# Kernel tuning notes

Measured on AMD Instinct MI355X. Metric: run time of the kernel, lower is better.

The kernel has to match this reference:

```python
import jax, jax.numpy as jnp
import numpy as np
from jax import lax

H = 1024
E = 8
TOP_K = 2


def setup_inputs() -> dict:
    key = jax.random.key(0)
    kx, k1, k2 = jax.random.split(key, 3)
    x = jax.random.normal(kx, (8, 2048, H), dtype=jnp.float32)
    # router MLP params, init normal(0, 0.02), zero bias (matches _init_weights)
    w1 = jax.random.normal(k1, (H, 2 * H), dtype=jnp.float32) * 0.02
    b1 = jnp.zeros((2 * H,), dtype=jnp.float32)
    w2 = jax.random.normal(k2, (2 * H, E), dtype=jnp.float32) * 0.02
    b2 = jnp.zeros((E,), dtype=jnp.float32)
    return {"x": x, "w1": w1, "b1": b1, "w2": w2, "b2": b2}


def reference(x, w1, b1, w2, b2):
    # gating MLP: Linear -> GELU (exact, torch default) -> Linear
    h = jax.nn.gelu(jnp.einsum('bsh,hf->bsf', x, w1) + b1, approximate=False)
    expert_weights = jnp.einsum('bsf,fe->bse', h, w2) + b2  # [B,S,E]

    top_k_weights, top_k_indices = lax.top_k(expert_weights, TOP_K)  # [B,S,K]
    top_k_weights = jax.nn.softmax(top_k_weights, axis=-1)

    # scatter renormalized weights into dense [B,S,E] mask (indices distinct -> one-hot sum)
    onehot = jax.nn.one_hot(top_k_indices, E, dtype=expert_weights.dtype)  # [B,S,K,E]
    masks = jnp.einsum('bsk,bske->bse', top_k_weights, onehot)

    expert_usage = masks.sum(axis=(0, 1))
    expert_usage = expert_usage / expert_usage.sum()
    target_usage = jnp.full_like(expert_usage, 1.0 / E)
    load_balancing_loss = jnp.mean((expert_usage - target_usage) ** 2)

    sparsity_loss = jnp.mean(jnp.sum(masks > 0, axis=-1).astype(jnp.float32)) / TOP_K
    total_loss = load_balancing_loss + 0.1 * sparsity_loss

    return expert_weights, masks, total_loss, expert_usage
```

## Files before the change

kernel.cpp:

```cpp
#include <hip/hip_runtime.h>
#include <math.h>

#define HDIM 1024
#define FDIM 2048
#define NEXP 8
#define MTOK 16384
#define NSLC 32
#define BM 128
#define BN 128

typedef __attribute__((ext_vector_type(8))) short bf16x8;
typedef __attribute__((ext_vector_type(4))) float f32x4;

__device__ inline unsigned short f2bf_rne(float f) {
    unsigned int u = __float_as_uint(f);
    u = (u + 0x7FFFu + ((u >> 16) & 1u)) >> 16;
    return (unsigned short)u;
}
__device__ inline float bf2f(unsigned short h) {
    unsigned int u = ((unsigned int)h) << 16;
    return __uint_as_float(u);
}

__global__ __launch_bounds__(256) void cvt_x(const float* __restrict__ x,
                                             unsigned short* __restrict__ af)
{
    __shared__ unsigned short hs[16384];
    __shared__ unsigned short ls[16384];
    const int mt = blockIdx.x;
    const float* src = x + (size_t)mt * 16384;
    const int m = threadIdx.x & 15;
    const int kseg = threadIdx.x >> 4;

    #pragma unroll
    for (int c = 0; c < 8; c++) {
        int k = c * 128 + kseg * 8;
        float v[8];
        *(float4*)(v)     = *(const float4*)(src + m * 1024 + k);
        *(float4*)(v + 4) = *(const float4*)(src + m * 1024 + k + 4);
        union { unsigned short u[8]; uint4 q; } oh, ol;
        #pragma unroll
        for (int j = 0; j < 8; j++) {
            unsigned short h = f2bf_rne(v[j]);
            oh.u[j] = h;
            ol.u[j] = f2bf_rne(v[j] - bf2f(h));
        }
        int kb = k >> 5, q = (k >> 3) & 3;
        int o = kb * 512 + m * 32 + q * 8;
        *(uint4*)(hs + o) = oh.q;
        *(uint4*)(ls + o) = ol.q;
    }
    __syncthreads();
    unsigned short* dst = af + (size_t)mt * 32768;
    #pragma unroll
    for (int c = 0; c < 16; c++) {
        int f = c * 2048 + threadIdx.x * 8;
        int kb = f >> 10, half = (f >> 9) & 1, idx = f & 511;
        int q = idx >> 7, mm = (idx >> 3) & 15;
        const unsigned short* s = (half ? ls : hs) + kb * 512 + mm * 32 + q * 8;
        *(uint4*)(dst + f) = *(const uint4*)s;
    }
}

__global__ __launch_bounds__(256) void cvt_w1f(const float* __restrict__ w1,
                                               unsigned short* __restrict__ wf)
{
    __shared__ float t[32][33];
    int n0 = blockIdx.x * 32;
    int k0 = blockIdx.y * 32;
    int lx = threadIdx.x & 31, ly = threadIdx.x >> 5;
    #pragma unroll
    for (int r = 0; r < 32; r += 8)
        t[ly + r][lx] = w1[(size_t)(k0 + ly + r) * FDIM + n0 + lx];
    __syncthreads();
    #pragma unroll
    for (int r = 0; r < 32; r += 8) {
        float v = t[lx][ly + r];
        unsigned short h = f2bf_rne(v);
        unsigned short l = f2bf_rne(v - bf2f(h));
        int n = n0 + ly + r, k = k0 + lx;
        size_t base = (size_t)((n >> 4) * 32 + (k >> 5)) * 1024;
        int lj = (((k >> 3) & 3) * 16 + (n & 15)) * 8 + (k & 7);
        wf[base + lj] = h;
        wf[base + 512 + lj] = l;
    }
}

__global__ __launch_bounds__(256, 2) void gemm1_mfma(
    const unsigned short* __restrict__ af, const unsigned short* __restrict__ wf,
    const float* __restrict__ b1, const float* __restrict__ w2,
    float* __restrict__ part)
{
    const int tid  = threadIdx.x;
    const int lane = tid & 63;
    const int l15  = lane & 15;
    const int q    = lane >> 4;
    const int wave = tid >> 6;
    const int wm   = wave & 1;
    const int wn   = wave >> 1;

    const int id = blockIdx.x;
    const int xcd = id & 7, seq = id >> 3;
    const int strip = seq >> 6;
    const int bn = (seq >> 2) & 15;
    const int bmo = seq & 3;
    const int bm = strip * 32 + xcd * 4 + bmo;
    const int m0 = bm * BM, n0 = bn * BN;

    const unsigned short* apt[4];
    const unsigned short* bpt[4];
    #pragma unroll
    for (int i = 0; i < 4; i++) {
        apt[i] = af + ((size_t)(bm * 8 + wm * 4 + i) * 32) * 1024 + lane * 8;
        bpt[i] = wf + ((size_t)(bn * 8 + wn * 4 + i) * 32) * 1024 + lane * 8;
    }

    f32x4 acc[4][4];
    #pragma unroll
    for (int i = 0; i < 4; i++)
        #pragma unroll
        for (int j = 0; j < 4; j++) acc[i][j] = (f32x4){0.f, 0.f, 0.f, 0.f};

    bf16x8 Ah0[4], Al0[4], Bh0[4], Bl0[4];
    bf16x8 Ah1[4], Al1[4], Bh1[4], Bl1[4];

    #pragma unroll
    for (int i = 0; i < 4; i++) {
        Ah0[i] = *(const bf16x8*)(apt[i]);
        Al0[i] = *(const bf16x8*)(apt[i] + 512);
        Bh0[i] = *(const bf16x8*)(bpt[i]);
        Bl0[i] = *(const bf16x8*)(bpt[i] + 512);
    }

    #pragma unroll 1
    for (int t = 0; t < 32; t += 2) {
        #pragma unroll
        for (int i = 0; i < 4; i++) {
            Ah1[i] = *(const bf16x8*)(apt[i] + 1024);
            Al1[i] = *(const bf16x8*)(apt[i] + 1536);
            Bh1[i] = *(const bf16x8*)(bpt[i] + 1024);
            Bl1[i] = *(const bf16x8*)(bpt[i] + 1536);
        }
        #pragma unroll
        for (int i = 0; i < 4; i++)
            #pragma unroll
            for (int j = 0; j < 4; j++) {
                acc[i][j] = __builtin_amdgcn_mfma_f32_16x16x32_bf16(
                    Ah0[i], Bh0[j], acc[i][j], 0, 0, 0);
                acc[i][j] = __builtin_amdgcn_mfma_f32_16x16x32_bf16(
                    Ah0[i], Bl0[j], acc[i][j], 0, 0, 0);
                acc[i][j] = __builtin_amdgcn_mfma_f32_16x16x32_bf16(
                    Al0[i], Bh0[j], acc[i][j], 0, 0, 0);
            }
        #pragma unroll
        for (int i = 0; i < 4; i++) { apt[i] += 2048; bpt[i] += 2048; }
        if (t + 2 < 32) {
            #pragma unroll
            for (int i = 0; i < 4; i++) {
                Ah0[i] = *(const bf16x8*)(apt[i]);
                Al0[i] = *(const bf16x8*)(apt[i] + 512);
                Bh0[i] = *(const bf16x8*)(bpt[i]);
                Bl0[i] = *(const bf16x8*)(bpt[i] + 512);
            }
        }
        #pragma unroll
        for (int i = 0; i < 4; i++)
            #pragma unroll
            for (int j = 0; j < 4; j++) {
                acc[i][j] = __builtin_amdgcn_mfma_f32_16x16x32_bf16(
                    Ah1[i], Bh1[j], acc[i][j], 0, 0, 0);
                acc[i][j] = __builtin_amdgcn_mfma_f32_16x16x32_bf16(
                    Ah1[i], Bl1[j], acc[i][j], 0, 0, 0);
                acc[i][j] = __builtin_amdgcn_mfma_f32_16x16x32_bf16(
                    Al1[i], Bh1[j], acc[i][j], 0, 0, 0);
            }
    }

    #pragma unroll
    for (int j = 0; j < 4; j++) {
        int n = n0 + wn * 64 + j * 16 + l15;
        float bb = b1[n];
        #pragma unroll
        for (int i = 0; i < 4; i++)
            #pragma unroll
            for (int r = 0; r < 4; r++) {
                float v = acc[i][j][r] + bb;
                acc[i][j][r] = 0.5f * v * (1.0f + erff(v * 0.70710678118654752f));
            }
    }

    float w2r[4][8];
    #pragma unroll
    for (int j = 0; j < 4; j++) {
        const float4* p = (const float4*)(w2 + (size_t)(n0 + wn * 64 + j * 16 + l15) * NEXP);
        float4 u = p[0], v = p[1];
        w2r[j][0] = u.x; w2r[j][1] = u.y; w2r[j][2] = u.z; w2r[j][3] = u.w;
        w2r[j][4] = v.x; w2r[j][5] = v.y; w2r[j][6] = v.z; w2r[j][7] = v.w;
    }

    const int sl = bn * 2 + wn;
    #pragma unroll
    for (int e = 0; e < NEXP; e++) {
        float p[4][4];
        #pragma unroll
        for (int i = 0; i < 4; i++)
            #pragma unroll
            for (int r = 0; r < 4; r++) {
                float s = 0.f;
                #pragma unroll
                for (int j = 0; j < 4; j++) s += acc[i][j][r] * w2r[j][e];
                p[i][r] = s;
            }
        #pragma unroll
        for (int off = 1; off < 16; off <<= 1)
            #pragma unroll
            for (int i = 0; i < 4; i++)
                #pragma unroll
                for (int r = 0; r < 4; r++)
                    p[i][r] += __shfl_xor(p[i][r], off);
        if (l15 == 0) {
            #pragma unroll
            for (int i = 0; i < 4; i++)
                #pragma unroll
                for (int r = 0; r < 4; r++) {
                    int m = m0 + wm * 64 + i * 16 + q * 4 + r;
                    part[(size_t)sl * (MTOK * NEXP) + (size_t)m * NEXP + e] = p[i][r];
                }
        }
    }
}

__global__ __launch_bounds__(256) void router_topk(
    const float* __restrict__ part, const float* __restrict__ b2,
    float* __restrict__ out, float* __restrict__ gu, int* __restrict__ gc)
{
    const int t = blockIdx.x * 256 + threadIdx.x;

    float logit[8];
    #pragma unroll
    for (int e = 0; e < 8; e++) logit[e] = b2[e];
    #pragma unroll
    for (int j = 0; j < NSLC; j++) {
        const float4* p4 = (const float4*)(part + (size_t)j * (MTOK * NEXP) + (size_t)t * NEXP);
        float4 u = p4[0], v = p4[1];
        logit[0] += u.x; logit[1] += u.y; logit[2] += u.z; logit[3] += u.w;
        logit[4] += v.x; logit[5] += v.y; logit[6] += v.z; logit[7] += v.w;
    }

    int i1 = 0; float v1 = logit[0];
    #pragma unroll
    for (int e = 1; e < 8; e++) { if (logit[e] > v1) { v1 = logit[e]; i1 = e; } }
    int i2 = -1; float v2 = -INFINITY;
    #pragma unroll
    for (int e = 0; e < 8; e++) {
        if (e != i1 && logit[e] > v2) { v2 = logit[e]; i2 = e; }
    }
    float ex = expf(v2 - v1);
    float inv = 1.0f / (1.0f + ex);
    float wa = inv, wb = ex * inv;

    float4* o = (float4*)(out + (size_t)t * NEXP);
    o[0] = make_float4(logit[0], logit[1], logit[2], logit[3]);
    o[1] = make_float4(logit[4], logit[5], logit[6], logit[7]);

    float mk[8];
    #pragma unroll
    for (int e = 0; e < 8; e++) mk[e] = 0.0f;
    mk[i1] = wa; mk[i2] = wb;
    float4* om = (float4*)(out + (size_t)(MTOK * NEXP) + (size_t)t * NEXP);
    om[0] = make_float4(mk[0], mk[1], mk[2], mk[3]);
    om[1] = make_float4(mk[4], mk[5], mk[6], mk[7]);

    __shared__ float us[8];
    __shared__ int cs;
    if (threadIdx.x < 8) us[threadIdx.x] = 0.0f;
    if (threadIdx.x == 0) cs = 0;
    __syncthreads();
    atomicAdd(&us[i1], wa);
    atomicAdd(&us[i2], wb);
    int cnt = (wa > 0.0f ? 1 : 0) + (wb > 0.0f ? 1 : 0);
    atomicAdd(&cs, cnt);
    __syncthreads();
    if (threadIdx.x < 8) atomicAdd(&gu[threadIdx.x], us[threadIdx.x]);
    if (threadIdx.x == 0) atomicAdd(gc, cs);
}

__global__ void router_final(const float* __restrict__ gu, const int* __restrict__ gc,
                             float* __restrict__ out)
{
    if (blockIdx.x == 0 && threadIdx.x == 0) {
        float u[8]; float tot = 0.0f;
        for (int e = 0; e < 8; e++) { u[e] = gu[e]; tot += u[e]; }
        float lb = 0.0f;
        for (int e = 0; e < 8; e++) {
            float un = u[e] / tot;
            out[2 * MTOK * NEXP + 1 + e] = un;
            float d = un - 0.125f;
            lb += d * d;
        }
        lb *= (1.0f / 8.0f);
        float sp = ((float)(*gc) / (float)MTOK) * 0.5f;
        out[2 * MTOK * NEXP] = lb + 0.1f * sp;
    }
}

extern "C" void kernel_launch(void* const* d_in, const int* in_sizes, int n_in,
                              void* d_out, int out_size, void* d_ws, size_t ws_size,
                              hipStream_t stream) {
    const float* x  = (const float*)d_in[0];
    const float* w1 = (const float*)d_in[1];
    const float* b1 = (const float*)d_in[2];
    const float* w2 = (const float*)d_in[3];
    const float* b2 = (const float*)d_in[4];
    float* out = (float*)d_out;

    unsigned short* af = (unsigned short*)d_ws;
    unsigned short* wf = af + (size_t)1024 * 32768;
    float* part = (float*)(wf + (size_t)128 * 32 * 1024);
    float* gu = part + (size_t)NSLC * MTOK * NEXP;
    int* gc = (int*)(gu + 8);

    hipMemsetAsync(gu, 0, 64, stream);

    cvt_x<<<1024, 256, 0, stream>>>(x, af);
    cvt_w1f<<<dim3(FDIM / 32, HDIM / 32), 256, 0, stream>>>(w1, wf);
    gemm1_mfma<<<2048, 256, 0, stream>>>(af, wf, b1, w2, part);
    router_topk<<<MTOK / 256, 256, 0, stream>>>(part, b2, out, gu, gc);
    router_final<<<1, 64, 0, stream>>>(gu, gc, out);
}
```

Before: 343.2 us.

## Stage GEMM tiles through LDS with a triple-buffered async global_load_lds pipeline

The gate GEMM moves from per-wave direct global-to-register loads to block-wide async global_load_lds copies into a three-stage LDS ring. Tiles grow to 256x128, with 512 threads and 8 waves per block. Every operand tile is now fetched once per block and shared by all waves, which cuts redundant global and L2 traffic and overlaps loads with MFMA work. The cost is about 144KB of dynamic LDS, which allows only one block per CU, plus barriers on every k-step and a setprio hint.

```diff
diff --git a/kernel.cpp b/kernel.cpp
--- a/kernel.cpp
+++ b/kernel.cpp
@@ -6,8 +6,8 @@
 #define NEXP 8
 #define MTOK 16384
 #define NSLC 32
-#define BM 128
-#define BN 128
+#define LDSB 24576
+#define LDS_BYTES (3 * 49152)
 
 typedef __attribute__((ext_vector_type(8))) short bf16x8;
 typedef __attribute__((ext_vector_type(4))) float f32x4;
@@ -86,33 +86,42 @@
     }
 }
 
-__global__ __launch_bounds__(256, 2) void gemm1_mfma(
+#define GLDX4(gp, lofs) __builtin_amdgcn_global_load_lds( \
+    (const __attribute__((address_space(1))) unsigned int*)(uintptr_t)(gp), \
+    (__attribute__((address_space(3))) unsigned int*)(unsigned int)(uintptr_t)(smem + (lofs)), \
+    16, 0, 0)
+
+__global__ __launch_bounds__(512, 2) void gemm1_mfma(
     const unsigned short* __restrict__ af, const unsigned short* __restrict__ wf,
     const float* __restrict__ b1, const float* __restrict__ w2,
     float* __restrict__ part)
 {
+    extern __shared__ unsigned short smem[];
     const int tid  = threadIdx.x;
     const int lane = tid & 63;
     const int l15  = lane & 15;
     const int q    = lane >> 4;
     const int wave = tid >> 6;
-    const int wm   = wave & 1;
-    const int wn   = wave >> 1;
-
-    const int id = blockIdx.x;
+    const int wm   = wave >> 1;
+    const int wn   = wave & 1;
+
+    const int id  = blockIdx.x;
     const int xcd = id & 7, seq = id >> 3;
-    const int strip = seq >> 6;
-    const int bn = (seq >> 2) & 15;
-    const int bmo = seq & 3;
-    const int bm = strip * 32 + xcd * 4 + bmo;
-    const int m0 = bm * BM, n0 = bn * BN;
-
-    const unsigned short* apt[4];
-    const unsigned short* bpt[4];
-    #pragma unroll
-    for (int i = 0; i < 4; i++) {
-        apt[i] = af + ((size_t)(bm * 8 + wm * 4 + i) * 32) * 1024 + lane * 8;
-        bpt[i] = wf + ((size_t)(bn * 8 + wn * 4 + i) * 32) * 1024 + lane * 8;
+    const int bn  = seq & 15;
+    const int bm  = xcd * 8 + (seq >> 4);
+    const int m0  = bm * 256, n0g = bn * 128;
+
+    const unsigned short* gb[6];
+    int lo[6];
+    #pragma unroll
+    for (int s = 0; s < 6; s++) {
+        int c = wave * 6 + s;
+        int f = c >> 1, half = c & 1;
+        const unsigned short* base = (f < 16)
+            ? af + (size_t)(bm * 16 + f) * 32768
+            : wf + (size_t)(bn * 8 + (f - 16)) * 32768;
+        gb[s] = base + half * 512 + lane * 8;
+        lo[s] = f * 1024 + half * 512;
     }
 
     f32x4 acc[4][4];
@@ -121,64 +130,58 @@
         #pragma unroll
         for (int j = 0; j < 4; j++) acc[i][j] = (f32x4){0.f, 0.f, 0.f, 0.f};
 
-    bf16x8 Ah0[4], Al0[4], Bh0[4], Bl0[4];
-    bf16x8 Ah1[4], Al1[4], Bh1[4], Bl1[4];
-
-    #pragma unroll
-    for (int i = 0; i < 4; i++) {
-        Ah0[i] = *(const bf16x8*)(apt[i]);
-        Al0[i] = *(const bf16x8*)(apt[i] + 512);
-        Bh0[i] = *(const bf16x8*)(bpt[i]);
-        Bl0[i] = *(const bf16x8*)(bpt[i] + 512);
-    }
-
+    #pragma unroll
+    for (int s = 0; s < 6; s++) GLDX4(gb[s], lo[s]);
+    #pragma unroll
+    for (int s = 0; s < 6; s++) GLDX4(gb[s] + 1024, LDSB + lo[s]);
+    asm volatile("s_waitcnt vmcnt(6)\n\ts_barrier" ::: "memory");
+
+    int bo = 0;
     #pragma unroll 1
-    for (int t = 0; t < 32; t += 2) {
-        #pragma unroll
-        for (int i = 0; i < 4; i++) {
-            Ah1[i] = *(const bf16x8*)(apt[i] + 1024);
-            Al1[i] = *(const bf16x8*)(apt[i] + 1536);
-            Bh1[i] = *(const bf16x8*)(bpt[i] + 1024);
-            Bl1[i] = *(const bf16x8*)(bpt[i] + 1536);
-        }
-        #pragma unroll
-        for (int i = 0; i < 4; i++)
-            #pragma unroll
-            for (int j = 0; j < 4; j++) {
-                acc[i][j] = __builtin_amdgcn_mfma_f32_16x16x32_bf16(
-                    Ah0[i], Bh0[j], acc[i][j], 0, 0, 0);
-                acc[i][j] = __builtin_amdgcn_mfma_f32_16x16x32_bf16(
-                    Ah0[i], Bl0[j], acc[i][j], 0, 0, 0);
-                acc[i][j] = __builtin_amdgcn_mfma_f32_16x16x32_bf16(
-                    Al0[i], Bh0[j], acc[i][j], 0, 0, 0);
+    for (int t = 0; t < 32; t++) {
+        int bi = bo + 2 * LDSB; if (bi >= 3 * LDSB) bi -= 3 * LDSB;
+        if (t + 2 < 32) {
+            #pragma unroll
+            for (int s = 0; s < 6; s++)
+                GLDX4(gb[s] + (size_t)(t + 2) * 1024, bi + lo[s]);
+        }
+        const unsigned short* sb = smem + bo;
+        bf16x8 Bh[4], Bl[4];
+        #pragma unroll
+        for (int j = 0; j < 4; j++) {
+            Bh[j] = *(const bf16x8*)(sb + (16 + wn * 4 + j) * 1024 + lane * 8);
+            Bl[j] = *(const bf16x8*)(sb + (16 + wn * 4 + j) * 1024 + 512 + lane * 8);
+        }
+        __builtin_amdgcn_s_setprio(1);
+        #pragma unroll
+        for (int ih = 0; ih < 2; ih++) {
+            bf16x8 Ah[2], Al[2];
+            #pragma unroll
+            for (int i = 0; i < 2; i++) {
+                int mt = wm * 4 + ih * 2 + i;
+                Ah[i] = *(const bf16x8*)(sb + mt * 1024 + lane * 8);
+                Al[i] = *(const bf16x8*)(sb + mt * 1024 + 512 + lane * 8);
             }
-        #pragma unroll
-        for (int i = 0; i < 4; i++) { apt[i] += 2048; bpt[i] += 2048; }
-        if (t + 2 < 32) {
-            #pragma unroll
-            for (int i = 0; i < 4; i++) {
-                Ah0[i] = *(const bf16x8*)(apt[i]);
-                Al0[i] = *(const bf16x8*)(apt[i] + 512);
-                Bh0[i] = *(const bf16x8*)(bpt[i]);
-                Bl0[i] = *(const bf16x8*)(bpt[i] + 512);
-            }
-        }
-        #pragma unroll
-        for (int i = 0; i < 4; i++)
-            #pragma unroll
-            for (int j = 0; j < 4; j++) {
-                acc[i][j] = __builtin_amdgcn_mfma_f32_16x16x32_bf16(
-                    Ah1[i], Bh1[j], acc[i][j], 0, 0, 0);
-                acc[i][j] = __builtin_amdgcn_mfma_f32_16x16x32_bf16(
-                    Ah1[i], Bl1[j], acc[i][j], 0, 0, 0);
-                acc[i][j] = __builtin_amdgcn_mfma_f32_16x16x32_bf16(
-                    Al1[i], Bh1[j], acc[i][j], 0, 0, 0);
-            }
+            #pragma unroll
+            for (int i = 0; i < 2; i++)
+                #pragma unroll
+                for (int j = 0; j < 4; j++) {
+                    f32x4 a = acc[ih * 2 + i][j];
+                    a = __builtin_amdgcn_mfma_f32_16x16x32_bf16(Ah[i], Bh[j], a, 0, 0, 0);
+                    a = __builtin_amdgcn_mfma_f32_16x16x32_bf16(Ah[i], Bl[j], a, 0, 0, 0);
+                    a = __builtin_amdgcn_mfma_f32_16x16x32_bf16(Al[i], Bh[j], a, 0, 0, 0);
+                    acc[ih * 2 + i][j] = a;
+                }
+        }
+        __builtin_amdgcn_s_setprio(0);
+        bo += LDSB; if (bo >= 3 * LDSB) bo -= 3 * LDSB;
+        if (t < 30)       asm volatile("s_waitcnt vmcnt(6)\n\ts_barrier" ::: "memory");
+        else if (t == 30) asm volatile("s_waitcnt vmcnt(0)\n\ts_barrier" ::: "memory");
     }
 
     #pragma unroll
     for (int j = 0; j < 4; j++) {
-        int n = n0 + wn * 64 + j * 16 + l15;
+        int n = n0g + wn * 64 + j * 16 + l15;
         float bb = b1[n];
         #pragma unroll
         for (int i = 0; i < 4; i++)
@@ -192,7 +195,7 @@
     float w2r[4][8];
     #pragma unroll
     for (int j = 0; j < 4; j++) {
-        const float4* p = (const float4*)(w2 + (size_t)(n0 + wn * 64 + j * 16 + l15) * NEXP);
+        const float4* p = (const float4*)(w2 + (size_t)(n0g + wn * 64 + j * 16 + l15) * NEXP);
         float4 u = p[0], v = p[1];
         w2r[j][0] = u.x; w2r[j][1] = u.y; w2r[j][2] = u.z; w2r[j][3] = u.w;
         w2r[j][4] = v.x; w2r[j][5] = v.y; w2r[j][6] = v.z; w2r[j][7] = v.w;
@@ -320,11 +323,18 @@
     float* gu = part + (size_t)NSLC * MTOK * NEXP;
     int* gc = (int*)(gu + 8);
 
+    static bool attr_done = false;
+    if (!attr_done) {
+        hipFuncSetAttribute((const void*)gemm1_mfma,
+                            hipFuncAttributeMaxDynamicSharedMemorySize, LDS_BYTES);
+        attr_done = true;
+    }
+
     hipMemsetAsync(gu, 0, 64, stream);
 
     cvt_x<<<1024, 256, 0, stream>>>(x, af);
     cvt_w1f<<<dim3(FDIM / 32, HDIM / 32), 256, 0, stream>>>(w1, wf);
-    gemm1_mfma<<<2048, 256, 0, stream>>>(af, wf, b1, w2, part);
+    gemm1_mfma<<<1024, 512, LDS_BYTES, stream>>>(af, wf, b1, w2, part);
     router_topk<<<MTOK / 256, 256, 0, stream>>>(part, b2, out, gu, gc);
     router_final<<<1, 64, 0, stream>>>(gu, gc, out);
 }
```

New measurement: 360.5 us. 1.05x slower.

## Cut operand register footprint in split-bf16 GEMM to raise occupancy to three blocks

Applied to the files above, without the earlier changes.

The main loop no longer double-buffers the low-half bf16 operands. It keeps a single Al/Bl buffer that is reloaded just before use, and reorders the MFMAs so all hi*hi products run before the cross terms. The launch bound rises from 2 to 3 blocks per CU, which fits the smaller register set and gives more waves to hide latency. In exchange, the low-half loads have less time to arrive before their MFMAs need them, which may expose global load latency.

```diff
diff --git a/kernel.cpp b/kernel.cpp
--- a/kernel.cpp
+++ b/kernel.cpp
@@ -86,7 +86,7 @@
     }
 }
 
-__global__ __launch_bounds__(256, 2) void gemm1_mfma(
+__global__ __launch_bounds__(256, 3) void gemm1_mfma(
     const unsigned short* __restrict__ af, const unsigned short* __restrict__ wf,
     const float* __restrict__ b1, const float* __restrict__ w2,
     float* __restrict__ part)
@@ -121,59 +121,72 @@
         #pragma unroll
         for (int j = 0; j < 4; j++) acc[i][j] = (f32x4){0.f, 0.f, 0.f, 0.f};
 
-    bf16x8 Ah0[4], Al0[4], Bh0[4], Bl0[4];
-    bf16x8 Ah1[4], Al1[4], Bh1[4], Bl1[4];
+    bf16x8 Ah0[4], Bh0[4];
+    bf16x8 Ah1[4], Bh1[4];
+    bf16x8 Al[4],  Bl[4];
 
     #pragma unroll
     for (int i = 0; i < 4; i++) {
         Ah0[i] = *(const bf16x8*)(apt[i]);
-        Al0[i] = *(const bf16x8*)(apt[i] + 512);
         Bh0[i] = *(const bf16x8*)(bpt[i]);
-        Bl0[i] = *(const bf16x8*)(bpt[i] + 512);
     }
 
     #pragma unroll 1
     for (int t = 0; t < 32; t += 2) {
         #pragma unroll
         for (int i = 0; i < 4; i++) {
+            Al[i] = *(const bf16x8*)(apt[i] + 512);
+            Bl[i] = *(const bf16x8*)(bpt[i] + 512);
+        }
+        #pragma unroll
+        for (int i = 0; i < 4; i++) {
             Ah1[i] = *(const bf16x8*)(apt[i] + 1024);
-            Al1[i] = *(const bf16x8*)(apt[i] + 1536);
             Bh1[i] = *(const bf16x8*)(bpt[i] + 1024);
-            Bl1[i] = *(const bf16x8*)(bpt[i] + 1536);
-        }
+        }
+        #pragma unroll
+        for (int i = 0; i < 4; i++)
+            #pragma unroll
+            for (int j = 0; j < 4; j++)
+                acc[i][j] = __builtin_amdgcn_mfma_f32_16x16x32_bf16(
+                    Ah0[i], Bh0[j], acc[i][j], 0, 0, 0);
         #pragma unroll
         for (int i = 0; i < 4; i++)
             #pragma unroll
             for (int j = 0; j < 4; j++) {
                 acc[i][j] = __builtin_amdgcn_mfma_f32_16x16x32_bf16(
-                    Ah0[i], Bh0[j], acc[i][j], 0, 0, 0);
-                acc[i][j] = __builtin_amdgcn_mfma_f32_16x16x32_bf16(
-                    Ah0[i], Bl0[j], acc[i][j], 0, 0, 0);
-                acc[i][j] = __builtin_amdgcn_mfma_f32_16x16x32_bf16(
-                    Al0[i], Bh0[j], acc[i][j], 0, 0, 0);
+                    Ah0[i], Bl[j], acc[i][j], 0, 0, 0);
+                acc[i][j] = __builtin_amdgcn_mfma_f32_16x16x32_bf16(
+                    Al[i], Bh0[j], acc[i][j], 0, 0, 0);
+            }
+        #pragma unroll
+        for (int i = 0; i < 4; i++) {
+            Al[i] = *(const bf16x8*)(apt[i] + 1536);
+            Bl[i] = *(const bf16x8*)(bpt[i] + 1536);
+        }
+        if (t + 2 < 32) {
+            #pragma unroll
+            for (int i = 0; i < 4; i++) {
+                Ah0[i] = *(const bf16x8*)(apt[i] + 2048);
+                Bh0[i] = *(const bf16x8*)(bpt[i] + 2048);
+            }
+        }
+        #pragma unroll
+        for (int i = 0; i < 4; i++)
+            #pragma unroll
+            for (int j = 0; j < 4; j++)
+                acc[i][j] = __builtin_amdgcn_mfma_f32_16x16x32_bf16(
+                    Ah1[i], Bh1[j], acc[i][j], 0, 0, 0);
+        #pragma unroll
+        for (int i = 0; i < 4; i++)
+            #pragma unroll
+            for (int j = 0; j < 4; j++) {
+                acc[i][j] = __builtin_amdgcn_mfma_f32_16x16x32_bf16(
+                    Ah1[i], Bl[j], acc[i][j], 0, 0, 0);
+                acc[i][j] = __builtin_amdgcn_mfma_f32_16x16x32_bf16(
+                    Al[i], Bh1[j], acc[i][j], 0, 0, 0);
             }
         #pragma unroll
         for (int i = 0; i < 4; i++) { apt[i] += 2048; bpt[i] += 2048; }
-        if (t + 2 < 32) {
-            #pragma unroll
-            for (int i = 0; i < 4; i++) {
-                Ah0[i] = *(const bf16x8*)(apt[i]);
-                Al0[i] = *(const bf16x8*)(apt[i] + 512);
-                Bh0[i] = *(const bf16x8*)(bpt[i]);
-                Bl0[i] = *(const bf16x8*)(bpt[i] + 512);
-            }
-        }
-        #pragma unroll
-        for (int i = 0; i < 4; i++)
-            #pragma unroll
-            for (int j = 0; j < 4; j++) {
-                acc[i][j] = __builtin_amdgcn_mfma_f32_16x16x32_bf16(
-                    Ah1[i], Bh1[j], acc[i][j], 0, 0, 0);
-                acc[i][j] = __builtin_amdgcn_mfma_f32_16x16x32_bf16(
-                    Ah1[i], Bl1[j], acc[i][j], 0, 0, 0);
-                acc[i][j] = __builtin_amdgcn_mfma_f32_16x16x32_bf16(
-                    Al1[i], Bh1[j], acc[i][j], 0, 0, 0);
-            }
     }
 
     #pragma unroll
```

Result: slower. 383.2 us (+11.6%).

## Enlarge GEMM1 block tile to 256x128 with interleaved A-fragment streaming

Applied to the files above, without the earlier changes.

The GEMM block tile in M doubles from 128 to 256 rows, so each wave holds 8x4 accumulators and every loaded B fragment feeds twice as many MFMAs. The grid halves to 1024 blocks and the block-to-XCD mapping changes. The K loop is rescheduled so A fragments stream in pairs, interleaved with MFMA groups, while B fragments for the next k-step are prefetched, which keeps register pressure bounded. The goal is to cut global/L2 load traffic per MFMA, at the cost of more accumulator registers (a risk to the two-blocks-per-SIMD occupancy target) and fewer blocks to balance across CUs.

```diff
diff --git a/kernel.cpp b/kernel.cpp
--- a/kernel.cpp
+++ b/kernel.cpp
@@ -6,8 +6,6 @@
 #define NEXP 8
 #define MTOK 16384
 #define NSLC 32
-#define BM 128
-#define BN 128
 
 typedef __attribute__((ext_vector_type(8))) short bf16x8;
 typedef __attribute__((ext_vector_type(4))) float f32x4;
@@ -86,6 +84,34 @@
     }
 }
 
+#define LOADB(BH, BL, tt) do { \
+    _Pragma("unroll") \
+    for (int j_ = 0; j_ < 4; j_++) { \
+        const unsigned short* p_ = bbase + (size_t)j_ * 32768 + (size_t)(tt) * 1024; \
+        BH[j_] = *(const bf16x8*)(p_); \
+        BL[j_] = *(const bf16x8*)(p_ + 512); \
+    } } while (0)
+
+#define LOADA(AH, AL, ip, tt) do { \
+    _Pragma("unroll") \
+    for (int k_ = 0; k_ < 2; k_++) { \
+        const unsigned short* p_ = abase + (size_t)((ip) * 2 + k_) * 32768 + (size_t)(tt) * 1024; \
+        AH[k_] = *(const bf16x8*)(p_); \
+        AL[k_] = *(const bf16x8*)(p_ + 512); \
+    } } while (0)
+
+#define MFMA_PAIR(AH, AL, BH, BL, ip) do { \
+    _Pragma("unroll") \
+    for (int k_ = 0; k_ < 2; k_++) \
+        _Pragma("unroll") \
+        for (int j_ = 0; j_ < 4; j_++) { \
+            f32x4 a_ = acc[(ip) * 2 + k_][j_]; \
+            a_ = __builtin_amdgcn_mfma_f32_16x16x32_bf16(AH[k_], BH[j_], a_, 0, 0, 0); \
+            a_ = __builtin_amdgcn_mfma_f32_16x16x32_bf16(AH[k_], BL[j_], a_, 0, 0, 0); \
+            a_ = __builtin_amdgcn_mfma_f32_16x16x32_bf16(AL[k_], BH[j_], a_, 0, 0, 0); \
+            acc[(ip) * 2 + k_][j_] = a_; \
+        } } while (0)
+
 __global__ __launch_bounds__(256, 2) void gemm1_mfma(
     const unsigned short* __restrict__ af, const unsigned short* __restrict__ wf,
     const float* __restrict__ b1, const float* __restrict__ w2,
@@ -99,81 +125,49 @@
     const int wm   = wave & 1;
     const int wn   = wave >> 1;
 
-    const int id = blockIdx.x;
+    const int id  = blockIdx.x;
     const int xcd = id & 7, seq = id >> 3;
-    const int strip = seq >> 6;
-    const int bn = (seq >> 2) & 15;
-    const int bmo = seq & 3;
-    const int bm = strip * 32 + xcd * 4 + bmo;
-    const int m0 = bm * BM, n0 = bn * BN;
-
-    const unsigned short* apt[4];
-    const unsigned short* bpt[4];
-    #pragma unroll
-    for (int i = 0; i < 4; i++) {
-        apt[i] = af + ((size_t)(bm * 8 + wm * 4 + i) * 32) * 1024 + lane * 8;
-        bpt[i] = wf + ((size_t)(bn * 8 + wn * 4 + i) * 32) * 1024 + lane * 8;
-    }
-
-    f32x4 acc[4][4];
-    #pragma unroll
-    for (int i = 0; i < 4; i++)
+    const int bn  = seq & 15;
+    const int bm  = xcd * 8 + (seq >> 4);
+    const int m0  = bm * 256, n0 = bn * 128;
+
+    const unsigned short* abase = af + (size_t)(bm * 16 + wm * 8) * 32768 + lane * 8;
+    const unsigned short* bbase = wf + (size_t)(bn * 8 + wn * 4) * 32768 + lane * 8;
+
+    f32x4 acc[8][4];
+    #pragma unroll
+    for (int i = 0; i < 8; i++)
         #pragma unroll
         for (int j = 0; j < 4; j++) acc[i][j] = (f32x4){0.f, 0.f, 0.f, 0.f};
 
-    bf16x8 Ah0[4], Al0[4], Bh0[4], Bl0[4];
-    bf16x8 Ah1[4], Al1[4], Bh1[4], Bl1[4];
-
-    #pragma unroll
-    for (int i = 0; i < 4; i++) {
-        Ah0[i] = *(const bf16x8*)(apt[i]);
-        Al0[i] = *(const bf16x8*)(apt[i] + 512);
-        Bh0[i] = *(const bf16x8*)(bpt[i]);
-        Bl0[i] = *(const bf16x8*)(bpt[i] + 512);
-    }
+    bf16x8 BhA[4], BlA[4], BhB[4], BlB[4];
+    bf16x8 AhX[2], AlX[2], AhY[2], AlY[2];
+
+    LOADB(BhA, BlA, 0);
+    LOADA(AhX, AlX, 0, 0);
 
     #pragma unroll 1
     for (int t = 0; t < 32; t += 2) {
-        #pragma unroll
-        for (int i = 0; i < 4; i++) {
-            Ah1[i] = *(const bf16x8*)(apt[i] + 1024);
-            Al1[i] = *(const bf16x8*)(apt[i] + 1536);
-            Bh1[i] = *(const bf16x8*)(bpt[i] + 1024);
-            Bl1[i] = *(const bf16x8*)(bpt[i] + 1536);
+        LOADA(AhY, AlY, 1, t);
+        MFMA_PAIR(AhX, AlX, BhA, BlA, 0);
+        LOADA(AhX, AlX, 2, t);
+        MFMA_PAIR(AhY, AlY, BhA, BlA, 1);
+        LOADA(AhY, AlY, 3, t);
+        MFMA_PAIR(AhX, AlX, BhA, BlA, 2);
+        LOADB(BhB, BlB, t + 1);
+        LOADA(AhX, AlX, 0, t + 1);
+        MFMA_PAIR(AhY, AlY, BhA, BlA, 3);
+        LOADA(AhY, AlY, 1, t + 1);
+        MFMA_PAIR(AhX, AlX, BhB, BlB, 0);
+        LOADA(AhX, AlX, 2, t + 1);
+        MFMA_PAIR(AhY, AlY, BhB, BlB, 1);
+        LOADA(AhY, AlY, 3, t + 1);
+        MFMA_PAIR(AhX, AlX, BhB, BlB, 2);
+        if (t + 2 < 32) {
+            LOADB(BhA, BlA, t + 2);
+            LOADA(AhX, AlX, 0, t + 2);
         }
-        #pragma unroll
-        for (int i = 0; i < 4; i++)
-            #pragma unroll
-            for (int j = 0; j < 4; j++) {
-                acc[i][j] = __builtin_amdgcn_mfma_f32_16x16x32_bf16(
-                    Ah0[i], Bh0[j], acc[i][j], 0, 0, 0);
-                acc[i][j] = __builtin_amdgcn_mfma_f32_16x16x32_bf16(
-                    Ah0[i], Bl0[j], acc[i][j], 0, 0, 0);
-                acc[i][j] = __builtin_amdgcn_mfma_f32_16x16x32_bf16(
-                    Al0[i], Bh0[j], acc[i][j], 0, 0, 0);
-            }
-        #pragma unroll
-        for (int i = 0; i < 4; i++) { apt[i] += 2048; bpt[i] += 2048; }
-        if (t + 2 < 32) {
-            #pragma unroll
-            for (int i = 0; i < 4; i++) {
-                Ah0[i] = *(const bf16x8*)(apt[i]);
-                Al0[i] = *(const bf16x8*)(apt[i] + 512);
-                Bh0[i] = *(const bf16x8*)(bpt[i]);
-                Bl0[i] = *(const bf16x8*)(bpt[i] + 512);
-            }
-        }
-        #pragma unroll
-        for (int i = 0; i < 4; i++)
-            #pragma unroll
-            for (int j = 0; j < 4; j++) {
-                acc[i][j] = __builtin_amdgcn_mfma_f32_16x16x32_bf16(
-                    Ah1[i], Bh1[j], acc[i][j], 0, 0, 0);
-                acc[i][j] = __builtin_amdgcn_mfma_f32_16x16x32_bf16(
-                    Ah1[i], Bl1[j], acc[i][j], 0, 0, 0);
-                acc[i][j] = __builtin_amdgcn_mfma_f32_16x16x32_bf16(
-                    Al1[i], Bh1[j], acc[i][j], 0, 0, 0);
-            }
+        MFMA_PAIR(AhY, AlY, BhB, BlB, 3);
     }
 
     #pragma unroll
@@ -181,7 +175,7 @@
         int n = n0 + wn * 64 + j * 16 + l15;
         float bb = b1[n];
         #pragma unroll
-        for (int i = 0; i < 4; i++)
+        for (int i = 0; i < 8; i++)
             #pragma unroll
             for (int r = 0; r < 4; r++) {
                 float v = acc[i][j][r] + bb;
@@ -201,9 +195,9 @@
     const int sl = bn * 2 + wn;
     #pragma unroll
     for (int e = 0; e < NEXP; e++) {
-        float p[4][4];
-        #pragma unroll
-        for (int i = 0; i < 4; i++)
+        float p[8][4];
+        #pragma unroll
+        for (int i = 0; i < 8; i++)
             #pragma unroll
             for (int r = 0; r < 4; r++) {
                 float s = 0.f;
@@ -214,16 +208,16 @@
         #pragma unroll
         for (int off = 1; off < 16; off <<= 1)
             #pragma unroll
-            for (int i = 0; i < 4; i++)
+            for (int i = 0; i < 8; i++)
                 #pragma unroll
                 for (int r = 0; r < 4; r++)
                     p[i][r] += __shfl_xor(p[i][r], off);
         if (l15 == 0) {
             #pragma unroll
-            for (int i = 0; i < 4; i++)
+            for (int i = 0; i < 8; i++)
                 #pragma unroll
                 for (int r = 0; r < 4; r++) {
-                    int m = m0 + wm * 64 + i * 16 + q * 4 + r;
+                    int m = m0 + wm * 128 + i * 16 + q * 4 + r;
                     part[(size_t)sl * (MTOK * NEXP) + (size_t)m * NEXP + e] = p[i][r];
                 }
         }
@@ -324,7 +318,7 @@
 
     cvt_x<<<1024, 256, 0, stream>>>(x, af);
     cvt_w1f<<<dim3(FDIM / 32, HDIM / 32), 256, 0, stream>>>(w1, wf);
-    gemm1_mfma<<<2048, 256, 0, stream>>>(af, wf, b1, w2, part);
+    gemm1_mfma<<<1024, 256, 0, stream>>>(af, wf, b1, w2, part);
     router_topk<<<MTOK / 256, 256, 0, stream>>>(part, b2, out, gu, gc);
     router_final<<<1, 64, 0, stream>>>(gu, gc, out);
 }
```

Result: slower. 422.2 us (+23.0%).
